# Kernel optimization log

Hardware: AMD Instinct MI355X
Metric: run time of the kernel (lower is better)

The kernel has to match this reference:

```python
import jax, jax.numpy as jnp
import numpy as np

B, S, D, H = 4, 2048, 1024, 16
DK = D // H
FF = 2 * D


def _layer_norm(x, g, b, eps):
    mu = jnp.mean(x, axis=-1, keepdims=True)
    var = jnp.mean(jnp.square(x - mu), axis=-1, keepdims=True)
    return (x - mu) * jax.lax.rsqrt(var + eps) * g + b


def setup_inputs() -> dict:
    key = jax.random.key(0)
    ks = jax.random.split(key, 8)
    s = 1.0 / np.sqrt(D)
    return {
        "x": jax.random.normal(ks[0], (B, S, D), jnp.float32),
        "Wq": jax.random.normal(ks[1], (D, D), jnp.float32) * s,
        "Wk": jax.random.normal(ks[2], (D, D), jnp.float32) * s,
        "Wv": jax.random.normal(ks[3], (D, D), jnp.float32) * s,
        "Wo": jax.random.normal(ks[4], (D, D), jnp.float32) * s,
        "ln1_g": jnp.ones((D,), jnp.float32),
        "ln1_b": jnp.zeros((D,), jnp.float32),
        "fc1_w": jax.random.normal(ks[5], (D, FF), jnp.float32) * s,
        "fc1_b": jnp.zeros((FF,), jnp.float32),
        "fc2_w": jax.random.normal(ks[6], (FF, D), jnp.float32) * (1.0 / np.sqrt(FF)),
        "fc2_b": jnp.zeros((D,), jnp.float32),
        "ln2_g": jnp.ones((D,), jnp.float32),
        "ln2_b": jnp.zeros((D,), jnp.float32),
    }


def reference(x, Wq, Wk, Wv, Wo, ln1_g, ln1_b, fc1_w, fc1_b, fc2_w, fc2_b, ln2_g, ln2_b):
    # --- multi-head self-attention (pre-LN, residual) ---
    residual = x
    xn = _layer_norm(x, ln1_g, ln1_b, 1e-5)  # nn.LayerNorm default eps
    q = (xn @ Wq).reshape(B, S, H, DK)
    k = (xn @ Wk).reshape(B, S, H, DK)
    v = (xn @ Wv).reshape(B, S, H, DK)
    scores = jnp.einsum("bqhd,bkhd->bhqk", q, k) / jnp.sqrt(jnp.float32(DK))
    attn = jax.nn.softmax(scores, axis=-1)  # dropout p=0.0 -> identity
    out = jnp.einsum("bhqk,bkhd->bqhd", attn, v).reshape(B, S, D)
    out = out @ Wo + residual
    # --- residual feed-forward (pre-LN, eps=1e-6) ---
    h = _layer_norm(out, ln2_g, ln2_b, 1e-6)
    h = jax.nn.relu(h @ fc1_w + fc1_b)
    h = h @ fc2_w + fc2_b
    return out + h
```

## Files before the change

### kernel.cpp

```cpp
#include <hip/hip_runtime.h>

#define BB   4
#define SS   2048
#define DDIM 1024
#define HH   16
#define DKK  64
#define FFF  2048
#define NTOK (BB * SS)
#define QKVS 3072
#define SCALE_Q 0.18033688011112042f

typedef __bf16 bf16x8 __attribute__((ext_vector_type(8)));
typedef float floatx4 __attribute__((ext_vector_type(4)));

__device__ __forceinline__ unsigned short f2bf(float f) {
    union { float f; unsigned u; } v; v.f = f;
    unsigned r = v.u + 0x7fffu + ((v.u >> 16) & 1u);
    return (unsigned short)(r >> 16);
}

__device__ __forceinline__ unsigned pack_bf_trunc(float a, float b) {
    union { float f; unsigned u; } x, y; x.f = a; y.f = b;
    return __builtin_amdgcn_perm(y.u, x.u, 0x07060302u);
}

__device__ __forceinline__ bf16x8 as_frag(uint4 v) {
    union { uint4 u; bf16x8 f; } c; c.u = v; return c.f;
}

__device__ __forceinline__ void async_copy16(const unsigned short* g, unsigned short* l) {
    __builtin_amdgcn_global_load_lds(
        (const __attribute__((address_space(1))) void*)g,
        (__attribute__((address_space(3))) void*)l, 16, 0, 0);
}

__global__ __launch_bounds__(256) void transpose_all(
    const float* __restrict__ Wq, const float* __restrict__ Wk,
    const float* __restrict__ Wv, const float* __restrict__ Wo,
    const float* __restrict__ fc1, const float* __restrict__ fc2,
    unsigned short* __restrict__ wqkvT, unsigned short* __restrict__ woT,
    unsigned short* __restrict__ fc1T, unsigned short* __restrict__ fc2T) {
    __shared__ float tile[64][65];
    int t = blockIdx.x;
    const float* src; unsigned short* dst; int K, N, tl;
    if (t < 256)       { src = Wq;  dst = wqkvT;                       K = 1024; N = 1024; tl = t; }
    else if (t < 512)  { src = Wk;  dst = wqkvT + (size_t)1024 * 1024; K = 1024; N = 1024; tl = t - 256; }
    else if (t < 768)  { src = Wv;  dst = wqkvT + (size_t)2048 * 1024; K = 1024; N = 1024; tl = t - 512; }
    else if (t < 1024) { src = Wo;  dst = woT;                         K = 1024; N = 1024; tl = t - 768; }
    else if (t < 1536) { src = fc1; dst = fc1T;                        K = 1024; N = 2048; tl = t - 1024; }
    else               { src = fc2; dst = fc2T;                        K = 2048; N = 1024; tl = t - 1536; }
    int kt = K >> 6;
    int k0 = (tl & (kt - 1)) * 64, n0 = (tl / kt) * 64;
    int tid = threadIdx.x;
#pragma unroll
    for (int i = 0; i < 16; ++i) {
        int e = i * 256 + tid;
        int r = e >> 6, c = e & 63;
        tile[r][c] = src[(size_t)(k0 + r) * N + (n0 + c)];
    }
    __syncthreads();
#pragma unroll
    for (int i = 0; i < 16; ++i) {
        int e = i * 256 + tid;
        int r = e >> 6, c = e & 63;
        dst[(size_t)(n0 + r) * K + (k0 + c)] = f2bf(tile[c][r]);
    }
}

__device__ __forceinline__ float block_sum256(float s) {
#pragma unroll
    for (int o = 32; o > 0; o >>= 1) s += __shfl_xor(s, o);
    __shared__ float partial[4];
    int w = threadIdx.x >> 6;
    __syncthreads();
    if ((threadIdx.x & 63) == 0) partial[w] = s;
    __syncthreads();
    return partial[0] + partial[1] + partial[2] + partial[3];
}

__global__ __launch_bounds__(256) void layernorm_bf16(
    const float* __restrict__ x, const float* __restrict__ g,
    const float* __restrict__ b, unsigned short* __restrict__ out, float eps) {
    size_t row = blockIdx.x;
    const float* xr = x + row * DDIM;
    int tid = threadIdx.x;
    float4 v = *(const float4*)(xr + tid * 4);
    float mu = block_sum256(v.x + v.y + v.z + v.w) * (1.0f / DDIM);
    float dx = v.x - mu, dy = v.y - mu, dz = v.z - mu, dw = v.w - mu;
    float var = block_sum256(dx * dx + dy * dy + dz * dz + dw * dw) * (1.0f / DDIM);
    float rstd = rsqrtf(var + eps);
    int c = tid * 4;
    unsigned short* o = out + row * DDIM + c;
    o[0] = f2bf(dx * rstd * g[c + 0] + b[c + 0]);
    o[1] = f2bf(dy * rstd * g[c + 1] + b[c + 1]);
    o[2] = f2bf(dz * rstd * g[c + 2] + b[c + 2]);
    o[3] = f2bf(dw * rstd * g[c + 3] + b[c + 3]);
}

__global__ __launch_bounds__(256) void gemm_db(
    const unsigned short* __restrict__ A, const unsigned short* __restrict__ Bt,
    const float* __restrict__ bias, const float* __restrict__ resid,
    float* __restrict__ outf, unsigned short* __restrict__ outh,
    int M, int N, int K, int relu, int lda, int qcols) {
    __shared__ unsigned short As[2][128 * 32];
    __shared__ unsigned short Bs[2][128 * 32];
    int tid = threadIdx.x;
    int wave = tid >> 6, lane = tid & 63;
    int lr = lane & 15, quad = lane >> 4;
    int bid = blockIdx.x;
    int m0 = (bid & 63) * 128;
    int n0 = (bid >> 6) * 128;
    int wm = (wave >> 1) * 64, wn = (wave & 1) * 64;

    floatx4 acc[4][4];
#pragma unroll
    for (int i = 0; i < 4; ++i)
#pragma unroll
        for (int t = 0; t < 4; ++t)
#pragma unroll
            for (int r = 0; r < 4; ++r) acc[i][t][r] = 0.0f;

    int srow = tid >> 2;
    int scol = (tid & 3) * 8;
    const unsigned short* ag0 = A  + (size_t)(m0 + srow) * lda + scol;
    const unsigned short* ag1 = A  + (size_t)(m0 + srow + 64) * lda + scol;
    const unsigned short* bg0 = Bt + (size_t)(n0 + srow) * K + scol;
    const unsigned short* bg1 = Bt + (size_t)(n0 + srow + 64) * K + scol;
    int l0 = srow * 32 + scol;
    int l1 = (srow + 64) * 32 + scol;

    async_copy16(ag0, &As[0][l0]);
    async_copy16(ag1, &As[0][l1]);
    async_copy16(bg0, &Bs[0][l0]);
    async_copy16(bg1, &Bs[0][l1]);

    int cur = 0;
    for (int k0 = 0; k0 < K; k0 += 32) {
        __syncthreads();
        if (k0 + 32 < K) {
            int nb = cur ^ 1, kn = k0 + 32;
            async_copy16(ag0 + kn, &As[nb][l0]);
            async_copy16(ag1 + kn, &As[nb][l1]);
            async_copy16(bg0 + kn, &Bs[nb][l0]);
            async_copy16(bg1 + kn, &Bs[nb][l1]);
        }
        bf16x8 af[4], bfr[4];
#pragma unroll
        for (int i = 0; i < 4; ++i)
            af[i] = *(const bf16x8*)&As[cur][(wm + 16 * i + lr) * 32 + quad * 8];
#pragma unroll
        for (int t = 0; t < 4; ++t)
            bfr[t] = *(const bf16x8*)&Bs[cur][(wn + 16 * t + lr) * 32 + quad * 8];
#pragma unroll
        for (int i = 0; i < 4; ++i)
#pragma unroll
            for (int t = 0; t < 4; ++t)
                acc[i][t] = __builtin_amdgcn_mfma_f32_16x16x32_bf16(
                    af[i], bfr[t], acc[i][t], 0, 0, 0);
        cur ^= 1;
    }

#pragma unroll
    for (int i = 0; i < 4; ++i) {
#pragma unroll
        for (int t = 0; t < 4; ++t) {
            int col = n0 + wn + 16 * t + lr;
            float cs = (col < qcols) ? SCALE_Q : 1.0f;
#pragma unroll
            for (int r = 0; r < 4; ++r) {
                int row = m0 + wm + 16 * i + quad * 4 + r;
                float v = acc[i][t][r];
                if (bias)  v += bias[col];
                if (resid) v += resid[(size_t)row * N + col];
                if (relu)  v = fmaxf(v, 0.0f);
                v *= cs;
                size_t idx = (size_t)row * N + col;
                if (outf) outf[idx] = v;
                else      outh[idx] = f2bf(v);
            }
        }
    }
}

#define BAR8() asm volatile("s_barrier" ::: "memory")
#define WAIT_LGKM0() do { asm volatile("s_waitcnt lgkmcnt(0)" ::: "memory"); \
                          __builtin_amdgcn_sched_barrier(0); } while (0)

#define STAGE_A8(T, h) do { \
    const unsigned short* s_ = A + (size_t)(m0 + (h) * 128 + rowin) * lda + (T) * 64; \
    unsigned short* d_ = Asm + ((((T) & 1) << 14) + ((h) << 13) + sdst); \
    async_copy16(s_ + c0, d_); async_copy16(s_ + c1, d_ + 512); } while (0)

#define STAGE_B8(T, h) do { \
    const unsigned short* s_ = Bt + (size_t)(n0 + (h) * 128 + rowin) * (size_t)K + (T) * 64; \
    unsigned short* d_ = Bsm + ((((T) & 1) << 14) + ((h) << 13) + sdst); \
    async_copy16(s_ + c0, d_); async_copy16(s_ + c1, d_ + 512); } while (0)

#define READ_A4(P, ibase) \
    _Pragma("unroll") \
    for (int i = 0; i < 4; ++i) \
        _Pragma("unroll") \
        for (int kk = 0; kk < 2; ++kk) \
            a_f[i][kk] = *(const bf16x8*)&Asm[(P) + aoff + ((((ibase) + i) * 2 + kk) << 9)];

#define READ_B8(P) \
    _Pragma("unroll") \
    for (int t = 0; t < 4; ++t) \
        _Pragma("unroll") \
        for (int kk = 0; kk < 2; ++kk) \
            b_f[t][kk] = *(const bf16x8*)&Bsm[(P) + boff + ((t * 2 + kk) << 9)];

#define MFMA_Q(ilo, tlo) \
    _Pragma("unroll") \
    for (int i = 0; i < 4; ++i) \
        _Pragma("unroll") \
        for (int t = 0; t < 2; ++t) \
            _Pragma("unroll") \
            for (int kk = 0; kk < 2; ++kk) \
                acc[(ilo) + i][(tlo) + t] = __builtin_amdgcn_mfma_f32_16x16x32_bf16( \
                    a_f[i][kk], b_f[(tlo) + t][kk], acc[(ilo) + i][(tlo) + t], 0, 0, 0);

__global__ __launch_bounds__(512, 2) void gemm_8ph(
    const unsigned short* __restrict__ A, const unsigned short* __restrict__ Bt,
    const float* __restrict__ bias, unsigned short* __restrict__ outh,
    int M, int N, int K, int relu, int lda, int qcols) {
    __shared__ unsigned short Asm[32768];
    __shared__ unsigned short Bsm[32768];

    int tid = threadIdx.x;
    int w = tid >> 6, lane = tid & 63;
    int lr = lane & 15, quad = lane >> 4;

    int nwg = gridDim.x;
    int bid = blockIdx.x;
    int swz = (bid & 7) * (nwg >> 3) + (bid >> 3);
    int m0 = (swz & 31) << 8;
    int n0 = (swz >> 5) << 8;

    int rowin = (w << 4) + (lane >> 2);
    int q = (lane & 3) ^ ((lane >> 5) << 1);
    int c0 = q * 8, c1 = 32 + q * 8;
    int sdst = w << 10;

    int qsw8 = ((lane & 8) ? (quad ^ 2) : quad) * 8;
    int aoff = (w >> 2) * 8192 + lr * 32 + qsw8;
    int boff = ((w & 3) >> 1) * 8192 + ((w & 3) & 1) * 4096 + lr * 32 + qsw8;
    int wm = (w >> 2) * 128, wn = (w & 3) * 64;

    floatx4 acc[8][4];
#pragma unroll
    for (int i = 0; i < 8; ++i)
#pragma unroll
        for (int t = 0; t < 4; ++t)
#pragma unroll
            for (int r = 0; r < 4; ++r) acc[i][t][r] = 0.0f;

    int NT = K >> 6;

    STAGE_B8(0, 0); STAGE_B8(0, 1); STAGE_A8(0, 0); STAGE_A8(0, 1);
    STAGE_B8(1, 0); STAGE_B8(1, 1); STAGE_A8(1, 0);
    asm volatile("s_waitcnt vmcnt(4)" ::: "memory");
    BAR8();

    bf16x8 a_f[4][2], b_f[4][2];

    for (int T = 0; T < NT; T += 2) {
        READ_A4(0, 0);
        READ_B8(0);
        if (T + 1 < NT) STAGE_A8(T + 1, 1);
        BAR8(); WAIT_LGKM0();
        __builtin_amdgcn_s_setprio(1); MFMA_Q(0, 0); __builtin_amdgcn_s_setprio(0);
        BAR8();
        if (T + 2 < NT) STAGE_B8(T + 2, 0);
        BAR8();
        __builtin_amdgcn_s_setprio(1); MFMA_Q(0, 2); __builtin_amdgcn_s_setprio(0);
        BAR8();
        READ_A4(0, 4);
        if (T + 2 < NT) STAGE_B8(T + 2, 1);
        BAR8(); WAIT_LGKM0();
        __builtin_amdgcn_s_setprio(1); MFMA_Q(4, 0); __builtin_amdgcn_s_setprio(0);
        BAR8();
        if (T + 2 < NT) STAGE_A8(T + 2, 0);
        BAR8();
        __builtin_amdgcn_s_setprio(1); MFMA_Q(4, 2); __builtin_amdgcn_s_setprio(0);
        if (T + 2 < NT) { asm volatile("s_waitcnt vmcnt(6)" ::: "memory"); }
        else            { asm volatile("s_waitcnt vmcnt(0)" ::: "memory"); }
        BAR8();

        READ_A4(16384, 0);
        READ_B8(16384);
        if (T + 2 < NT) STAGE_A8(T + 2, 1);
        BAR8(); WAIT_LGKM0();
        __builtin_amdgcn_s_setprio(1); MFMA_Q(0, 0); __builtin_amdgcn_s_setprio(0);
        BAR8();
        if (T + 3 < NT) STAGE_B8(T + 3, 0);
        BAR8();
        __builtin_amdgcn_s_setprio(1); MFMA_Q(0, 2); __builtin_amdgcn_s_setprio(0);
        BAR8();
        READ_A4(16384, 4);
        if (T + 3 < NT) STAGE_B8(T + 3, 1);
        BAR8(); WAIT_LGKM0();
        __builtin_amdgcn_s_setprio(1); MFMA_Q(4, 0); __builtin_amdgcn_s_setprio(0);
        BAR8();
        if (T + 3 < NT) STAGE_A8(T + 3, 0);
        BAR8();
        __builtin_amdgcn_s_setprio(1); MFMA_Q(4, 2); __builtin_amdgcn_s_setprio(0);
        if (T + 3 < NT) { asm volatile("s_waitcnt vmcnt(6)" ::: "memory"); }
        else            { asm volatile("s_waitcnt vmcnt(0)" ::: "memory"); }
        BAR8();
    }

#pragma unroll
    for (int i = 0; i < 8; ++i) {
#pragma unroll
        for (int t = 0; t < 4; ++t) {
            int col = n0 + wn + 16 * t + lr;
            float cs = (col < qcols) ? SCALE_Q : 1.0f;
            float bv = bias ? bias[col] : 0.0f;
#pragma unroll
            for (int r = 0; r < 4; ++r) {
                int row = m0 + wm + 16 * i + quad * 4 + r;
                float v = acc[i][t][r] + bv;
                if (relu) v = fmaxf(v, 0.0f);
                outh[(size_t)row * N + col] = f2bf(v * cs);
            }
        }
    }
}

__global__ __launch_bounds__(256) void transpose_v(
    const unsigned short* __restrict__ vsrc, unsigned short* __restrict__ vt) {
    int bh = blockIdx.y;
    int b = bh >> 4, h = bh & 15;
    int s = blockIdx.x * 256 + threadIdx.x;
    size_t inbase = ((size_t)(b * SS + s)) * QKVS + h * 64;
    size_t outbase = (size_t)bh * 64 * SS;
    int sp = (s & ~63) + 4 * (s & 15) + ((s >> 4) & 3);
#pragma unroll
    for (int dk8 = 0; dk8 < 8; ++dk8) {
        uint4 raw = *(const uint4*)(vsrc + inbase + dk8 * 8);
        const unsigned short* ph = (const unsigned short*)&raw;
#pragma unroll
        for (int i = 0; i < 8; ++i)
            vt[outbase + (size_t)(dk8 * 8 + i) * SS + sp] = ph[i];
    }
}

#define PST 68

__global__ __launch_bounds__(256, 2) void attention_mfma10(
    const unsigned short* __restrict__ qkv, const unsigned short* __restrict__ vt,
    unsigned short* __restrict__ ctx ) {
    __shared__ unsigned short Ps[256 * PST];

    int tid = threadIdx.x;
    int wave = tid >> 6, lane = tid & 63;
    int lr = lane & 15, quad = lane >> 4;
    int wq = wave >> 1, wj = wave & 1;

    int bid = blockIdx.x;
    int bh = bid & 63;
    int qt = bid >> 6;
    int b = bh >> 4, h = bh & 15;
    int q0 = qt * 128;
    size_t q_base = ((size_t)b * SS) * QKVS + h * 64;
    size_t k_base = q_base + 1024;
    size_t vt_base = (size_t)bh * 64 * SS;

    uint4 af[4][2];
#pragma unroll
    for (int i = 0; i < 4; ++i)
#pragma unroll
        for (int kk = 0; kk < 2; ++kk)
            af[i][kk] = *(const uint4*)(qkv + q_base +
                (size_t)(q0 + 64 * wq + 16 * i + lr) * QKVS + kk * 32 + quad * 8);

    floatx4 o[4][4];
    float l[4][4];
#pragma unroll
    for (int i = 0; i < 4; ++i)
#pragma unroll
        for (int t = 0; t < 4; ++t) {
#pragma unroll
            for (int r = 0; r < 4; ++r) o[i][t][r] = 0.0f;
            l[i][t] = 0.0f;
        }
    floatx4 zf;
#pragma unroll
    for (int r = 0; r < 4; ++r) zf[r] = 0.0f;

    unsigned short* myPs = &Ps[wave * 64 * PST];

    for (int jt = 0; jt < SS / 128; ++jt) {
        int j0 = jt * 128 + 64 * wj;

        floatx4 s[4][4];
        {
            uint4 bv[4];
#pragma unroll
            for (int t = 0; t < 4; ++t)
                bv[t] = *(const uint4*)(qkv + k_base +
                    (size_t)(j0 + 16 * t + lr) * QKVS + quad * 8);
            __builtin_amdgcn_s_setprio(1);
#pragma unroll
            for (int i = 0; i < 4; ++i)
#pragma unroll
                for (int t = 0; t < 4; ++t)
                    s[i][t] = __builtin_amdgcn_mfma_f32_16x16x32_bf16(
                        as_frag(af[i][0]), as_frag(bv[t]), zf, 0, 0, 0);
            __builtin_amdgcn_s_setprio(0);
        }
        {
            uint4 bv[4];
#pragma unroll
            for (int t = 0; t < 4; ++t)
                bv[t] = *(const uint4*)(qkv + k_base +
                    (size_t)(j0 + 16 * t + lr) * QKVS + 32 + quad * 8);
            __builtin_amdgcn_s_setprio(1);
#pragma unroll
            for (int i = 0; i < 4; ++i)
#pragma unroll
                for (int t = 0; t < 4; ++t)
                    s[i][t] = __builtin_amdgcn_mfma_f32_16x16x32_bf16(
                        as_frag(af[i][1]), as_frag(bv[t]), s[i][t], 0, 0, 0);
            __builtin_amdgcn_s_setprio(0);
        }

#pragma unroll
        for (int i = 0; i < 4; ++i) {
#pragma unroll
            for (int r = 0; r < 4; ++r) {
                float p0 = exp2f(s[i][0][r]);
                float p1 = exp2f(s[i][1][r]);
                float p2 = exp2f(s[i][2][r]);
                float p3 = exp2f(s[i][3][r]);
                l[i][r] += (p0 + p1) + (p2 + p3);
                uint2 w;
                w.x = pack_bf_trunc(p0, p1);
                w.y = pack_bf_trunc(p2, p3);
                *(uint2*)&myPs[(16 * i + quad * 4 + r) * PST + 4 * lr] = w;
            }
        }

#pragma unroll
        for (int kk = 0; kk < 2; ++kk) {
            uint4 vv[4];
#pragma unroll
            for (int t = 0; t < 4; ++t)
                vv[t] = *(const uint4*)(vt + vt_base +
                    (size_t)(16 * t + lr) * SS + j0 + kk * 32 + quad * 8);
            bf16x8 pf[4];
#pragma unroll
            for (int i = 0; i < 4; ++i)
                pf[i] = *(const bf16x8*)&myPs[(16 * i + lr) * PST + kk * 32 + quad * 8];
            __builtin_amdgcn_s_setprio(1);
#pragma unroll
            for (int i = 0; i < 4; ++i)
#pragma unroll
                for (int t = 0; t < 4; ++t)
                    o[i][t] = __builtin_amdgcn_mfma_f32_16x16x32_bf16(
                        pf[i], as_frag(vv[t]), o[i][t], 0, 0, 0);
            __builtin_amdgcn_s_setprio(0);
        }
    }

#pragma unroll
    for (int i = 0; i < 4; ++i)
#pragma unroll
        for (int r = 0; r < 4; ++r) {
            float ls = l[i][r];
            ls += __shfl_xor(ls, 1);
            ls += __shfl_xor(ls, 2);
            ls += __shfl_xor(ls, 4);
            ls += __shfl_xor(ls, 8);
            l[i][r] = ls;
        }

    __syncthreads();
    float* obuf = (float*)Ps;
    float* lbuf = obuf + 2 * 64 * 65;
    if (wj == 1) {
#pragma unroll
        for (int i = 0; i < 4; ++i)
#pragma unroll
            for (int r = 0; r < 4; ++r) {
                int rl = 16 * i + quad * 4 + r;
#pragma unroll
                for (int t = 0; t < 4; ++t)
                    obuf[(wq * 64 + rl) * 65 + 16 * t + lr] = o[i][t][r];
                if (lr == 0) lbuf[wq * 64 + rl] = l[i][r];
            }
    }
    __syncthreads();
    if (wj == 0) {
#pragma unroll
        for (int i = 0; i < 4; ++i)
#pragma unroll
            for (int r = 0; r < 4; ++r) {
                int rl = 16 * i + quad * 4 + r;
                float inv = 1.0f / (l[i][r] + lbuf[wq * 64 + rl]);
                int row = q0 + 64 * wq + rl;
                size_t base = ((size_t)(b * SS + row)) * QKVS + h * 64;
#pragma unroll
                for (int t = 0; t < 4; ++t)
                    ctx[base + 16 * t + lr] =
                        f2bf((o[i][t][r] + obuf[(wq * 64 + rl) * 65 + 16 * t + lr]) * inv);
            }
    }
}

extern "C" void kernel_launch(void* const* d_in, const int* in_sizes, int n_in,
                              void* d_out, int out_size, void* d_ws, size_t ws_size,
                              hipStream_t stream) {
    const float* x     = (const float*)d_in[0];
    const float* Wq    = (const float*)d_in[1];
    const float* Wk    = (const float*)d_in[2];
    const float* Wv    = (const float*)d_in[3];
    const float* Wo    = (const float*)d_in[4];
    const float* ln1g  = (const float*)d_in[5];
    const float* ln1b  = (const float*)d_in[6];
    const float* fc1w  = (const float*)d_in[7];
    const float* fc1b  = (const float*)d_in[8];
    const float* fc2w  = (const float*)d_in[9];
    const float* fc2b  = (const float*)d_in[10];
    const float* ln2g  = (const float*)d_in[11];
    const float* ln2b  = (const float*)d_in[12];
    float* out = (float*)d_out;

    char* ws = (char*)d_ws;
    const size_t MB = 1024 * 1024;
    unsigned short* wqkvT = (unsigned short*)(ws + 0 * MB);
    unsigned short* woT   = (unsigned short*)(ws + 6 * MB);
    unsigned short* fc1T  = (unsigned short*)(ws + 8 * MB);
    unsigned short* fc2T  = (unsigned short*)(ws + 12 * MB);
    unsigned short* xn    = (unsigned short*)(ws + 16 * MB);
    unsigned short* vt    = xn;
    unsigned short* hn    = xn;
    unsigned short* qkvb  = (unsigned short*)(ws + 32 * MB);
    unsigned short* ctx   = qkvb + 2048;
    unsigned short* h1    = qkvb;

    dim3 blk(256);

    transpose_all<<<2048, blk, 0, stream>>>(Wq, Wk, Wv, Wo, fc1w, fc2w,
                                            wqkvT, woT, fc1T, fc2T);

    layernorm_bf16<<<NTOK, blk, 0, stream>>>(x, ln1g, ln1b, xn, 1e-5f);

    gemm_8ph<<<384, 512, 0, stream>>>(xn, wqkvT, nullptr, qkvb,
                                      NTOK, QKVS, 1024, 0, 1024, 1024);
    transpose_v<<<dim3(8, 64), blk, 0, stream>>>(qkvb + 2048, vt);

    attention_mfma10<<<1024, blk, 0, stream>>>(qkvb, vt, ctx);

    gemm_db<<<512, blk, 0, stream>>>(ctx, woT, nullptr, x, out, nullptr,
                                     NTOK, 1024, 1024, 0, QKVS, 0);
    layernorm_bf16<<<NTOK, blk, 0, stream>>>(out, ln2g, ln2b, hn, 1e-6f);
    gemm_8ph<<<256, 512, 0, stream>>>(hn, fc1T, fc1b, h1,
                                      NTOK, 2048, 1024, 1, 1024, 0);
    gemm_db<<<512, blk, 0, stream>>>(h1, fc2T, fc2b, out, out, nullptr,
                                     NTOK, 1024, 2048, 0, 2048, 0);
}
```

Before: 525.2 us.

## Replace simple double-buffered GEMM with 8-wave phased pipelined GEMM for Wo and fc2

Removes the 256-thread double-buffered gemm_db kernel and adds gemm_8ph_b, a 512-thread 128x256-tile GEMM. It interleaves async global-to-LDS staging with quarter-sized MFMA groups, uses barriers and setprio, swizzles LDS columns, and remaps blocks for L2 locality. The output projection and fc2 GEMMs (fp32 output with residual add) now use it. This targets the memory-latency stalls and low MFMA utilisation of the old kernel, at the cost of more LDS per block and a more complex synchronisation schedule.

New measurement: 491.1 us. 1.07x faster.

```diff
diff --git a/kernel.cpp b/kernel.cpp
--- a/kernel.cpp
+++ b/kernel.cpp
@@ -97,91 +97,6 @@
     o[3] = f2bf(dw * rstd * g[c + 3] + b[c + 3]);
 }
 
-__global__ __launch_bounds__(256) void gemm_db(
-    const unsigned short* __restrict__ A, const unsigned short* __restrict__ Bt,
-    const float* __restrict__ bias, const float* __restrict__ resid,
-    float* __restrict__ outf, unsigned short* __restrict__ outh,
-    int M, int N, int K, int relu, int lda, int qcols) {
-    __shared__ unsigned short As[2][128 * 32];
-    __shared__ unsigned short Bs[2][128 * 32];
-    int tid = threadIdx.x;
-    int wave = tid >> 6, lane = tid & 63;
-    int lr = lane & 15, quad = lane >> 4;
-    int bid = blockIdx.x;
-    int m0 = (bid & 63) * 128;
-    int n0 = (bid >> 6) * 128;
-    int wm = (wave >> 1) * 64, wn = (wave & 1) * 64;
-
-    floatx4 acc[4][4];
-#pragma unroll
-    for (int i = 0; i < 4; ++i)
-#pragma unroll
-        for (int t = 0; t < 4; ++t)
-#pragma unroll
-            for (int r = 0; r < 4; ++r) acc[i][t][r] = 0.0f;
-
-    int srow = tid >> 2;
-    int scol = (tid & 3) * 8;
-    const unsigned short* ag0 = A  + (size_t)(m0 + srow) * lda + scol;
-    const unsigned short* ag1 = A  + (size_t)(m0 + srow + 64) * lda + scol;
-    const unsigned short* bg0 = Bt + (size_t)(n0 + srow) * K + scol;
-    const unsigned short* bg1 = Bt + (size_t)(n0 + srow + 64) * K + scol;
-    int l0 = srow * 32 + scol;
-    int l1 = (srow + 64) * 32 + scol;
-
-    async_copy16(ag0, &As[0][l0]);
-    async_copy16(ag1, &As[0][l1]);
-    async_copy16(bg0, &Bs[0][l0]);
-    async_copy16(bg1, &Bs[0][l1]);
-
-    int cur = 0;
-    for (int k0 = 0; k0 < K; k0 += 32) {
-        __syncthreads();
-        if (k0 + 32 < K) {
-            int nb = cur ^ 1, kn = k0 + 32;
-            async_copy16(ag0 + kn, &As[nb][l0]);
-            async_copy16(ag1 + kn, &As[nb][l1]);
-            async_copy16(bg0 + kn, &Bs[nb][l0]);
-            async_copy16(bg1 + kn, &Bs[nb][l1]);
-        }
-        bf16x8 af[4], bfr[4];
-#pragma unroll
-        for (int i = 0; i < 4; ++i)
-            af[i] = *(const bf16x8*)&As[cur][(wm + 16 * i + lr) * 32 + quad * 8];
-#pragma unroll
-        for (int t = 0; t < 4; ++t)
-            bfr[t] = *(const bf16x8*)&Bs[cur][(wn + 16 * t + lr) * 32 + quad * 8];
-#pragma unroll
-        for (int i = 0; i < 4; ++i)
-#pragma unroll
-            for (int t = 0; t < 4; ++t)
-                acc[i][t] = __builtin_amdgcn_mfma_f32_16x16x32_bf16(
-                    af[i], bfr[t], acc[i][t], 0, 0, 0);
-        cur ^= 1;
-    }
-
-#pragma unroll
-    for (int i = 0; i < 4; ++i) {
-#pragma unroll
-        for (int t = 0; t < 4; ++t) {
-            int col = n0 + wn + 16 * t + lr;
-            float cs = (col < qcols) ? SCALE_Q : 1.0f;
-#pragma unroll
-            for (int r = 0; r < 4; ++r) {
-                int row = m0 + wm + 16 * i + quad * 4 + r;
-                float v = acc[i][t][r];
-                if (bias)  v += bias[col];
-                if (resid) v += resid[(size_t)row * N + col];
-                if (relu)  v = fmaxf(v, 0.0f);
-                v *= cs;
-                size_t idx = (size_t)row * N + col;
-                if (outf) outf[idx] = v;
-                else      outh[idx] = f2bf(v);
-            }
-        }
-    }
-}
-
 #define BAR8() asm volatile("s_barrier" ::: "memory")
 #define WAIT_LGKM0() do { asm volatile("s_waitcnt lgkmcnt(0)" ::: "memory"); \
                           __builtin_amdgcn_sched_barrier(0); } while (0)
@@ -323,6 +238,149 @@
                 float v = acc[i][t][r] + bv;
                 if (relu) v = fmaxf(v, 0.0f);
                 outh[(size_t)row * N + col] = f2bf(v * cs);
+            }
+        }
+    }
+}
+
+#define STAGE_A1B(T, h) do { \
+    const unsigned short* s_ = A + (size_t)(m0 + (h) * 64 + rowA) * lda + (T) * 64 + colA; \
+    unsigned short* d_ = Asm + ((((T) & 1) << 13) + ((h) << 12) + (w << 9)); \
+    async_copy16(s_, d_); } while (0)
+
+#define STAGE_B8B(T, h) do { \
+    const unsigned short* s_ = Bt + (size_t)(n0 + (h) * 128 + rowin) * (size_t)K + (T) * 64; \
+    unsigned short* d_ = Bsm + ((((T) & 1) << 14) + ((h) << 13) + sdst); \
+    async_copy16(s_ + c0, d_); async_copy16(s_ + c1, d_ + 512); } while (0)
+
+#define READ_A4B(PA) \
+    _Pragma("unroll") \
+    for (int i = 0; i < 4; ++i) \
+        _Pragma("unroll") \
+        for (int kk = 0; kk < 2; ++kk) \
+            a_f[i][kk] = *(const bf16x8*)&Asm[(PA) + aoffb + ((i * 2 + kk) << 9)];
+
+#define READ_B8B(PB) \
+    _Pragma("unroll") \
+    for (int t = 0; t < 4; ++t) \
+        _Pragma("unroll") \
+        for (int kk = 0; kk < 2; ++kk) \
+            b_f[t][kk] = *(const bf16x8*)&Bsm[(PB) + boff + ((t * 2 + kk) << 9)];
+
+#define MFMA_QB(ilo, tlo) \
+    _Pragma("unroll") \
+    for (int i = 0; i < 2; ++i) \
+        _Pragma("unroll") \
+        for (int t = 0; t < 2; ++t) \
+            _Pragma("unroll") \
+            for (int kk = 0; kk < 2; ++kk) \
+                acc[(ilo) + i][(tlo) + t] = __builtin_amdgcn_mfma_f32_16x16x32_bf16( \
+                    a_f[(ilo) + i][kk], b_f[(tlo) + t][kk], acc[(ilo) + i][(tlo) + t], 0, 0, 0);
+
+__global__ __launch_bounds__(512, 2) void gemm_8ph_b(
+    const unsigned short* __restrict__ A, const unsigned short* __restrict__ Bt,
+    const float* __restrict__ bias, const float* __restrict__ resid,
+    float* __restrict__ outf, int M, int N, int K, int lda) {
+    __shared__ unsigned short Asm[16384];
+    __shared__ unsigned short Bsm[32768];
+
+    int tid = threadIdx.x;
+    int w = tid >> 6, lane = tid & 63;
+    int lr = lane & 15, quad = lane >> 4;
+
+    int nwg = gridDim.x;
+    int bid = blockIdx.x;
+    int swz = (bid & 7) * (nwg >> 3) + (bid >> 3);
+    int m0 = (swz & 63) << 7;
+    int n0 = (swz >> 6) << 8;
+
+    int rowin = (w << 4) + (lane >> 2);
+    int q = (lane & 3) ^ ((lane >> 5) << 1);
+    int c0 = q * 8, c1 = 32 + q * 8;
+    int sdst = w << 10;
+
+    int rowA = ((w >> 1) << 4) + (lane >> 2);
+    int colA = ((w & 1) << 5) + (((lane & 3) ^ ((lane & 32) ? 2 : 0)) << 3);
+
+    int qsw8 = ((lane & 8) ? (quad ^ 2) : quad) * 8;
+    int aoffb = ((w >> 2) << 12) + lr * 32 + qsw8;
+    int boff = ((w & 3) >> 1) * 8192 + ((w & 3) & 1) * 4096 + lr * 32 + qsw8;
+    int wm = (w >> 2) * 64, wn = (w & 3) * 64;
+
+    floatx4 acc[4][4];
+#pragma unroll
+    for (int i = 0; i < 4; ++i)
+#pragma unroll
+        for (int t = 0; t < 4; ++t)
+#pragma unroll
+            for (int r = 0; r < 4; ++r) acc[i][t][r] = 0.0f;
+
+    int NT = K >> 6;
+
+    STAGE_B8B(0, 0); STAGE_B8B(0, 1); STAGE_A1B(0, 0); STAGE_A1B(0, 1);
+    STAGE_B8B(1, 0); STAGE_B8B(1, 1); STAGE_A1B(1, 0);
+    asm volatile("s_waitcnt vmcnt(5)" ::: "memory");
+    BAR8();
+
+    bf16x8 a_f[4][2], b_f[4][2];
+
+    for (int T = 0; T < NT; T += 2) {
+        READ_A4B(0);
+        READ_B8B(0);
+        if (T + 1 < NT) STAGE_A1B(T + 1, 1);
+        BAR8(); WAIT_LGKM0();
+        __builtin_amdgcn_s_setprio(1); MFMA_QB(0, 0); __builtin_amdgcn_s_setprio(0);
+        BAR8();
+        if (T + 2 < NT) STAGE_B8B(T + 2, 0);
+        BAR8();
+        __builtin_amdgcn_s_setprio(1); MFMA_QB(0, 2); __builtin_amdgcn_s_setprio(0);
+        BAR8();
+        if (T + 2 < NT) STAGE_B8B(T + 2, 1);
+        BAR8();
+        __builtin_amdgcn_s_setprio(1); MFMA_QB(2, 0); __builtin_amdgcn_s_setprio(0);
+        BAR8();
+        if (T + 2 < NT) STAGE_A1B(T + 2, 0);
+        BAR8();
+        __builtin_amdgcn_s_setprio(1); MFMA_QB(2, 2); __builtin_amdgcn_s_setprio(0);
+        if (T + 2 < NT) { asm volatile("s_waitcnt vmcnt(5)" ::: "memory"); }
+        else            { asm volatile("s_waitcnt vmcnt(0)" ::: "memory"); }
+        BAR8();
+
+        READ_A4B(8192);
+        READ_B8B(16384);
+        if (T + 2 < NT) STAGE_A1B(T + 2, 1);
+        BAR8(); WAIT_LGKM0();
+        __builtin_amdgcn_s_setprio(1); MFMA_QB(0, 0); __builtin_amdgcn_s_setprio(0);
+        BAR8();
+        if (T + 3 < NT) STAGE_B8B(T + 3, 0);
+        BAR8();
+        __builtin_amdgcn_s_setprio(1); MFMA_QB(0, 2); __builtin_amdgcn_s_setprio(0);
+        BAR8();
+        if (T + 3 < NT) STAGE_B8B(T + 3, 1);
+        BAR8();
+        __builtin_amdgcn_s_setprio(1); MFMA_QB(2, 0); __builtin_amdgcn_s_setprio(0);
+        BAR8();
+        if (T + 3 < NT) STAGE_A1B(T + 3, 0);
+        BAR8();
+        __builtin_amdgcn_s_setprio(1); MFMA_QB(2, 2); __builtin_amdgcn_s_setprio(0);
+        if (T + 3 < NT) { asm volatile("s_waitcnt vmcnt(5)" ::: "memory"); }
+        else            { asm volatile("s_waitcnt vmcnt(0)" ::: "memory"); }
+        BAR8();
+    }
+
+#pragma unroll
+    for (int i = 0; i < 4; ++i) {
+#pragma unroll
+        for (int t = 0; t < 4; ++t) {
+            int col = n0 + wn + 16 * t + lr;
+            float bv = bias ? bias[col] : 0.0f;
+#pragma unroll
+            for (int r = 0; r < 4; ++r) {
+                int row = m0 + wm + 16 * i + quad * 4 + r;
+                size_t idx = (size_t)row * N + col;
+                float v = acc[i][t][r] + bv;
+                if (resid) v += resid[idx];
+                outf[idx] = v;
             }
         }
     }
@@ -553,11 +611,11 @@
 
     attention_mfma10<<<1024, blk, 0, stream>>>(qkvb, vt, ctx);
 
-    gemm_db<<<512, blk, 0, stream>>>(ctx, woT, nullptr, x, out, nullptr,
-                                     NTOK, 1024, 1024, 0, QKVS, 0);
+    gemm_8ph_b<<<256, 512, 0, stream>>>(ctx, woT, nullptr, x, out,
+                                        NTOK, 1024, 1024, QKVS);
     layernorm_bf16<<<NTOK, blk, 0, stream>>>(out, ln2g, ln2b, hn, 1e-6f);
     gemm_8ph<<<256, 512, 0, stream>>>(hn, fc1T, fc1b, h1,
                                       NTOK, 2048, 1024, 1, 1024, 0);
-    gemm_db<<<512, blk, 0, stream>>>(h1, fc2T, fc2b, out, out, nullptr,
-                                     NTOK, 1024, 2048, 0, 2048, 0);
-}
+    gemm_8ph_b<<<256, 512, 0, stream>>>(h1, fc2T, fc2b, out, out,
+                                        NTOK, 1024, 2048, 2048);
+}
```
